# Optimization experiments

Hardware: AMD Instinct MI355X
Metric: run time of the kernel (lower is better)

Reference implementation:

```python
import jax, jax.numpy as jnp
import numpy as np

C = 1.0                 # ball curvature magnitude (k = -c)
SQRT_C = float(np.sqrt(C))
MIN_NORM = 1e-15
BALL_EPS = 4e-3         # geoopt float32 projection eps


def _artanh(x):
    return jnp.arctanh(jnp.clip(x, -1.0 + 1e-7, 1.0 - 1e-7))


def _norm(x):
    return jnp.clip(jnp.linalg.norm(x, axis=-1, keepdims=True), MIN_NORM)


def expmap0(u):
    n = _norm(u)
    return jnp.tanh(SQRT_C * n) * u / (SQRT_C * n)


def logmap0(y):
    n = _norm(y)
    return _artanh(SQRT_C * n) * y / (SQRT_C * n)


def mobius_add(x, y):
    x2 = jnp.sum(x * x, axis=-1, keepdims=True)
    y2 = jnp.sum(y * y, axis=-1, keepdims=True)
    xy = jnp.sum(x * y, axis=-1, keepdims=True)
    num = (1.0 + 2.0 * C * xy + C * y2) * x + (1.0 - C * x2) * y
    den = 1.0 + 2.0 * C * xy + C * C * x2 * y2
    return num / jnp.clip(den, MIN_NORM)


def mobius_matvec(W, x):
    # x: [N, in], W: [out, in]
    mx = x @ W.T                                   # [N, out]
    xn = _norm(x)
    mxn = _norm(mx)
    res = jnp.tanh(mxn / xn * _artanh(SQRT_C * xn)) * mx / (mxn * SQRT_C)
    zero = jnp.linalg.norm(mx, axis=-1, keepdims=True) <= 1e-10
    return jnp.where(zero, jnp.zeros_like(res), res)


def project(x):
    n = _norm(x)
    maxnorm = (1.0 - BALL_EPS) / SQRT_C
    return jnp.where(n > maxnorm, x * (maxnorm / n), x)


def setup_inputs() -> dict:
    key = jax.random.key(0)
    k1, k2, k3, k4, k5 = jax.random.split(key, 5)
    N, E, D_IN, D_OUT = 100000, 600000, 128, 128
    x_h = jax.random.normal(k1, (N, D_IN), dtype=jnp.float32) * 0.05  # inside ball
    edge_index = jax.random.randint(k2, (2, E), 0, N, dtype=jnp.int64)
    edge_weight = jax.random.uniform(k3, (E,), dtype=jnp.float32)
    xav = float(np.sqrt(2.0 / (D_IN + D_OUT)))
    W = jax.random.normal(k4, (D_OUT, D_IN), dtype=jnp.float32) * xav
    b = jax.random.normal(k5, (D_OUT,), dtype=jnp.float32) * 0.01
    a = jnp.asarray(0.25, dtype=jnp.float32)  # PReLU slope
    return {"x_h": x_h, "edge_index": edge_index, "edge_weight": edge_weight,
            "W": W, "b": b, "a": a}


def reference(x_h, edge_index, edge_weight, W, b, a):
    N = x_h.shape[0]
    # HyperbolicLinear: mobius matvec + mobius bias add
    h = mobius_matvec(W, x_h)
    h = mobius_add(h, expmap0(b))
    # tangent-space aggregation
    h_t = logmap0(h)                                  # [N, D]
    src, dst = edge_index[0], edge_index[1]
    msg = h_t[src] * edge_weight[:, None]             # [E, D]
    agg = jax.ops.segment_sum(msg, dst, num_segments=N) + h_t
    # mobius PReLU activation
    h2_t = logmap0(expmap0(agg))
    h2_t = jnp.where(h2_t >= 0, h2_t, a * h2_t)
    return project(expmap0(h2_t))
```

## Files before the change

### kernel.cpp

```cpp
#include <hip/hip_runtime.h>
#include <hip/hip_fp16.h>
#include <cstdint>

#define D 128
#define BLK 256

constexpr float MINN    = 1e-15f;
constexpr float ATCLIP  = 1.0f - 1e-7f;
constexpr float BALLEPS = 4e-3f;

typedef _Float16 f16x8 __attribute__((ext_vector_type(8)));
typedef float    f32x4 __attribute__((ext_vector_type(4)));

union H4 { _Float16 h[4]; uint2 u2; };
union H8 { _Float16 h[8]; uint4 u4; };

__device__ __forceinline__ float red32(float v) {
    v += __shfl_xor(v, 1);
    v += __shfl_xor(v, 2);
    v += __shfl_xor(v, 4);
    v += __shfl_xor(v, 8);
    v += __shfl_xor(v, 16);
    return v;
}

__device__ __forceinline__ float red64(float v) {
    v += __shfl_xor(v, 1, 64);
    v += __shfl_xor(v, 2, 64);
    v += __shfl_xor(v, 4, 64);
    v += __shfl_xor(v, 8, 64);
    v += __shfl_xor(v, 16, 64);
    v += __shfl_xor(v, 32, 64);
    return v;
}

__device__ __forceinline__ float red16(float v) {
    v += __shfl_xor(v, 1, 64);
    v += __shfl_xor(v, 2, 64);
    v += __shfl_xor(v, 4, 64);
    v += __shfl_xor(v, 8, 64);
    return v;
}

__device__ __forceinline__ float tanh_fast(float x) {
    float e = __expf(2.f * fminf(x, 15.f));
    return __fdividef(e - 1.f, e + 1.f);
}
__device__ __forceinline__ float artanh_fast(float x) {
    x = fminf(x, ATCLIP);
    return 0.5f * __logf(__fdividef(1.f + x, 1.f - x));
}

__global__ __launch_bounds__(BLK) void k_node_mfma(
    const float* __restrict__ x, const float* __restrict__ W,
    const float* __restrict__ b, uint2* __restrict__ ht, int N,
    const int* __restrict__ ei, int* __restrict__ cnt, int E, int eslice)
{
    __shared__ _Float16 Ws[D * 136];
    __shared__ _Float16 xs[64 * 136];
    __shared__ float    ps[D];
    __shared__ float    xn2s[64];

    const int t     = threadIdx.x;
    const int node0 = blockIdx.x * 64;

    {
        int e0 = blockIdx.x * eslice;
        for (int i = t; i < eslice; i += BLK) {
            int e = e0 + i;
            if (e < E) atomicAdd(&cnt[ei[E + e]], 1);
        }
    }

    for (int it = 0; it < 16; ++it) {
        int lin = it * BLK + t;
        int row = lin >> 5;
        int c4  = (lin & 31) * 4;
        float4 v = ((const float4*)W)[lin];
        H4 u;
        u.h[0] = (_Float16)v.x; u.h[1] = (_Float16)v.y;
        u.h[2] = (_Float16)v.z; u.h[3] = (_Float16)v.w;
        *(uint2*)&Ws[row * 136 + c4] = u.u2;
    }

    for (int it = 0; it < 8; ++it) {
        int lin  = it * BLK + t;
        int node = lin >> 5;
        int c4   = (lin & 31) * 4;
        int gn   = node0 + node;
        float4 v = make_float4(0.f, 0.f, 0.f, 0.f);
        if (gn < N) v = ((const float4*)x)[(size_t)gn * 32 + (lin & 31)];
        H4 u;
        u.h[0] = (_Float16)v.x; u.h[1] = (_Float16)v.y;
        u.h[2] = (_Float16)v.z; u.h[3] = (_Float16)v.w;
        *(uint2*)&xs[node * 136 + c4] = u.u2;
        float s = fmaf(v.x, v.x, fmaf(v.y, v.y, fmaf(v.z, v.z, v.w * v.w)));
        s = red32(s);
        if ((t & 31) == 0) xn2s[node] = s;
    }

    {
        float2 b2 = ((const float2*)b)[t & 63];
        float pb  = fmaf(b2.x, b2.x, b2.y * b2.y);
        float bn2 = red64(pb);
        float bnc    = fmaxf(sqrtf(bn2), MINN);
        float bscale = __fdividef(tanh_fast(bnc), bnc);
        if (t < D) ps[t] = b[t] * bscale;
        xn2s[0] = xn2s[0];
        __syncthreads();
        const int lane = t & 63;
        const int w    = t >> 6;
        const int c    = lane & 15;
        const int g    = lane >> 4;
        const float y2 = bscale * bscale * bn2;

        f32x4 Cf[8];
#pragma unroll
        for (int mt = 0; mt < 8; ++mt) Cf[mt] = (f32x4){0.f, 0.f, 0.f, 0.f};

        const _Float16* xbase = &xs[(w * 16 + c) * 136];
#pragma unroll
        for (int s = 0; s < 4; ++s) {
            f16x8 Bf = *(const f16x8*)&xbase[s * 32 + g * 8];
#pragma unroll
            for (int mt = 0; mt < 8; ++mt) {
                f16x8 Af = *(const f16x8*)&Ws[(mt * 16 + c) * 136 + s * 32 + g * 8];
                Cf[mt] = __builtin_amdgcn_mfma_f32_16x16x32_f16(Af, Bf, Cf[mt], 0, 0, 0);
            }
        }

        float pm = 0.f, pd = 0.f;
        const float4* ps4 = (const float4*)ps;
#pragma unroll
        for (int mt = 0; mt < 8; ++mt) {
            float4 pv = ps4[mt * 4 + g];
            pm = fmaf(Cf[mt][0], Cf[mt][0], pm);
            pm = fmaf(Cf[mt][1], Cf[mt][1], pm);
            pm = fmaf(Cf[mt][2], Cf[mt][2], pm);
            pm = fmaf(Cf[mt][3], Cf[mt][3], pm);
            pd = fmaf(Cf[mt][0], pv.x, pd);
            pd = fmaf(Cf[mt][1], pv.y, pd);
            pd = fmaf(Cf[mt][2], pv.z, pd);
            pd = fmaf(Cf[mt][3], pv.w, pd);
        }
        pm += __shfl_xor(pm, 16); pm += __shfl_xor(pm, 32);
        pd += __shfl_xor(pd, 16); pd += __shfl_xor(pd, 32);
        float xn2 = xn2s[w * 16 + c];

        float xn      = fmaxf(sqrtf(xn2), MINN);
        float mxn_raw = sqrtf(pm);
        float mxn     = fmaxf(mxn_raw, MINN);
        float alpha   = __fdividef(tanh_fast(__fdividef(mxn, xn) * artanh_fast(xn)), mxn);
        if (mxn_raw <= 1e-10f) alpha = 0.f;

        float x2  = alpha * alpha * pm;
        float xy  = alpha * pd;
        float den = fmaxf(fmaf(x2, y2, 1.f + 2.f * xy), MINN);
        float ca  = __fdividef((1.f + 2.f * xy + y2) * alpha, den);
        float cb  = __fdividef(1.f - x2, den);

        float hn2 = ca * ca * pm + 2.f * ca * cb * pd + cb * cb * y2;
        float hn  = fmaxf(sqrtf(hn2), MINN);
        float lsc = __fdividef(artanh_fast(hn), hn);
        float s1  = lsc * ca, s2 = lsc * cb;

        uint2* lout = (uint2*)((char*)xs + (size_t)w * 16 * 136 * 2);
#pragma unroll
        for (int mt = 0; mt < 8; ++mt) {
            float4 pv = ps4[mt * 4 + g];
            H4 u;
            u.h[0] = (_Float16)fmaf(s1, Cf[mt][0], s2 * pv.x);
            u.h[1] = (_Float16)fmaf(s1, Cf[mt][1], s2 * pv.y);
            u.h[2] = (_Float16)fmaf(s1, Cf[mt][2], s2 * pv.z);
            u.h[3] = (_Float16)fmaf(s1, Cf[mt][3], s2 * pv.w);
            lout[c * 33 + mt * 4 + g] = u.u2;
        }
    }
    __syncthreads();

    for (int it = 0; it < 8; ++it) {
        int lin  = it * BLK + t;
        int node = lin >> 5;
        int col  = lin & 31;
        int gn   = node0 + node;
        if (gn < N) {
            const uint2* lsrc = (const uint2*)((const char*)xs + (size_t)(node >> 4) * 4352);
            ht[(size_t)gn * 32 + col] = lsrc[(node & 15) * 33 + col];
        }
    }
}

__global__ __launch_bounds__(256) void k_scan1(
    const int* __restrict__ cnt, int* __restrict__ ptr,
    int* __restrict__ part, int N)
{
    __shared__ int s[256];
    int t = threadIdx.x;
    int base = blockIdx.x * 1024 + t * 4;
    int v0 = 0, v1 = 0, v2 = 0, v3 = 0;
    if (base + 3 < N) {
        int4 q = *(const int4*)&cnt[base];
        v0 = q.x; v1 = q.y; v2 = q.z; v3 = q.w;
    } else {
        if (base + 0 < N) v0 = cnt[base + 0];
        if (base + 1 < N) v1 = cnt[base + 1];
        if (base + 2 < N) v2 = cnt[base + 2];
        if (base + 3 < N) v3 = cnt[base + 3];
    }
    int sum = v0 + v1 + v2 + v3;
    s[t] = sum;
    __syncthreads();
    for (int off = 1; off < 256; off <<= 1) {
        int xv = (t >= off) ? s[t - off] : 0;
        __syncthreads();
        s[t] += xv;
        __syncthreads();
    }
    int excl = s[t] - sum;
    if (t == 255) part[blockIdx.x] = s[255];
    int r = excl;
    if (base + 0 < N) ptr[base + 0] = r; r += v0;
    if (base + 1 < N) ptr[base + 1] = r; r += v1;
    if (base + 2 < N) ptr[base + 2] = r; r += v2;
    if (base + 3 < N) ptr[base + 3] = r;
}

__global__ __launch_bounds__(256) void k_scan2(int* __restrict__ part, int nc) {
    __shared__ int s[256];
    int t = threadIdx.x;
    int v = (t < nc) ? part[t] : 0;
    s[t] = v;
    __syncthreads();
    for (int off = 1; off < 256; off <<= 1) {
        int xv = (t >= off) ? s[t - off] : 0;
        __syncthreads();
        s[t] += xv;
        __syncthreads();
    }
    if (t < nc) part[t] = s[t] - v;
}

__global__ void k_scatter(const int* __restrict__ ei, const float* __restrict__ ew,
                          int* __restrict__ ptr, const int* __restrict__ part,
                          int2* __restrict__ sorted, int E)
{
    int e = blockIdx.x * 256 + threadIdx.x;
    if (e >= E) return;
    int src = ei[e];
    int dst = ei[E + e];
    float w = ew[e];
    int pos = atomicAdd(&ptr[dst], 1) + part[dst >> 10];
    sorted[pos] = make_int2(src << 8, __float_as_int(w));
}

__global__ __launch_bounds__(256) void k_agg_final(
    const char* __restrict__ htb, const int* __restrict__ ptr,
    const int* __restrict__ part, const int2* __restrict__ sorted,
    const float* __restrict__ a_in, float* __restrict__ out, int N)
{
    const int t   = threadIdx.x;
    const int li  = t & 15;
    const int grp = t >> 4;
    const int n   = blockIdx.x * 16 + grp;
    if (n >= N) return;
    const float a = a_in[0];

    H8 own; own.u4 = *(const uint4*)(htb + (size_t)n * 256 + li * 16);
    float acc[8];
#pragma unroll
    for (int k = 0; k < 8; ++k) acc[k] = (float)own.h[k];

    int s0 = (n > 0) ? (ptr[n - 1] + part[(n - 1) >> 10]) : 0;
    int e0 = ptr[n] + part[n >> 10];

    const int lioff = li * 16;
    int j = s0;
    for (; j + 2 <= e0; j += 2) {
        int2 d0 = sorted[j];
        int2 d1 = sorted[j + 1];
        H8 g0, g1;
        g0.u4 = *(const uint4*)(htb + (unsigned)d0.x + lioff);
        g1.u4 = *(const uint4*)(htb + (unsigned)d1.x + lioff);
        float w0 = __int_as_float(d0.y);
        float w1 = __int_as_float(d1.y);
#pragma unroll
        for (int k = 0; k < 8; ++k) acc[k] = fmaf((float)g0.h[k], w0, acc[k]);
#pragma unroll
        for (int k = 0; k < 8; ++k) acc[k] = fmaf((float)g1.h[k], w1, acc[k]);
    }
    if (j < e0) {
        int2 d = sorted[j];
        H8 g; g.u4 = *(const uint4*)(htb + (unsigned)d.x + lioff);
        float w = __int_as_float(d.y);
#pragma unroll
        for (int k = 0; k < 8; ++k) acc[k] = fmaf((float)g.h[k], w, acc[k]);
    }

    float pv = 0.f;
#pragma unroll
    for (int k = 0; k < 8; ++k) {
        float v = acc[k];
        v = (v >= 0.f) ? v : a * v;
        acc[k] = v;
        pv = fmaf(v, v, pv);
    }
    float m2 = red16(pv);
    float rc = fmaxf(sqrtf(m2), MINN);
    float te = tanh_fast(rc);
    const float maxn = 1.0f - BALLEPS;
    float fsc = __fdividef(fminf(fmaxf(te, MINN), maxn), rc);

    float4 o0 = make_float4(fsc * acc[0], fsc * acc[1], fsc * acc[2], fsc * acc[3]);
    float4 o1 = make_float4(fsc * acc[4], fsc * acc[5], fsc * acc[6], fsc * acc[7]);
    float4* orow = (float4*)(out + (size_t)n * D);
    orow[li * 2 + 0] = o0;
    orow[li * 2 + 1] = o1;
}

extern "C" void kernel_launch(void* const* d_in, const int* in_sizes, int n_in,
                              void* d_out, int out_size, void* d_ws, size_t ws_size,
                              hipStream_t stream)
{
    const float* x  = (const float*)d_in[0];
    const int*   ei = (const int*)  d_in[1];
    const float* ew = (const float*)d_in[2];
    const float* W  = (const float*)d_in[3];
    const float* b  = (const float*)d_in[4];
    const float* a  = (const float*)d_in[5];
    float* out = (float*)d_out;

    const int N = in_sizes[0] / D;
    const int E = in_sizes[1] / 2;

    char* ws = (char*)d_ws;
    size_t HT_B   = (size_t)N * D * 2;
    uint2* ht     = (uint2*)ws;
    int*   cnt    = (int*)(ws + HT_B);
    int*   ptr    = (int*)(ws + HT_B + (size_t)N * 4);
    int*   part   = (int*)(ws + HT_B + (size_t)N * 8);
    int2*  sorted = (int2*)(ws + HT_B + (size_t)N * 8 + 1024);

    int nc  = (N + 1023) / 1024;
    int nb1 = (N + 63) / 64;
    int eslice = (E + nb1 - 1) / nb1;

    hipMemsetAsync(cnt, 0, (size_t)N * 4, stream);
    k_node_mfma<<<nb1, BLK, 0, stream>>>(x, W, b, ht, N, ei, cnt, E, eslice);
    k_scan1<<<nc, 256, 0, stream>>>(cnt, ptr, part, N);
    k_scan2<<<1, 256, 0, stream>>>(part, nc);
    k_scatter<<<(E + 255) / 256, 256, 0, stream>>>(ei, ew, ptr, part, sorted, E);
    k_agg_final<<<(N + 15) / 16, 256, 0, stream>>>((const char*)ht, ptr, part, sorted, a, out, N);
}
```

Baseline: 228.6 us.

## Pre-convert W to fp16 in MFMA fragment layout and read it from global

Adds a small kernel that converts W to fp16 once per call, stored in the per-lane MFMA A-fragment order. The node kernel then stops staging W into LDS in every block and loads the A fragments straight from global memory, where they should stay cached in L2. This drops 34 KB of LDS per block, which may raise occupancy, and removes the repeated per-block convert and store. In exchange it adds an extra kernel launch and global loads inside the MFMA loop.

Result: faster. 220.9 us (-3.4%).

```diff
diff --git a/kernel.cpp b/kernel.cpp
--- a/kernel.cpp
+++ b/kernel.cpp
@@ -51,12 +51,26 @@
     return 0.5f * __logf(__fdividef(1.f + x, 1.f - x));
 }
 
+__global__ void k_wcvt(const float* __restrict__ W, _Float16* __restrict__ Wh) {
+    int i = blockIdx.x * 256 + threadIdx.x;
+    if (i >= 2048) return;
+    int f = i >> 7;
+    int r = i & 127;
+    const float4* src = (const float4*)(W + r * 128 + f * 8);
+    float4 v0 = src[0], v1 = src[1];
+    H8 u;
+    u.h[0] = (_Float16)v0.x; u.h[1] = (_Float16)v0.y;
+    u.h[2] = (_Float16)v0.z; u.h[3] = (_Float16)v0.w;
+    u.h[4] = (_Float16)v1.x; u.h[5] = (_Float16)v1.y;
+    u.h[6] = (_Float16)v1.z; u.h[7] = (_Float16)v1.w;
+    *(uint4*)(Wh + i * 8) = u.u4;
+}
+
 __global__ __launch_bounds__(BLK) void k_node_mfma(
-    const float* __restrict__ x, const float* __restrict__ W,
+    const float* __restrict__ x, const _Float16* __restrict__ Wh,
     const float* __restrict__ b, uint2* __restrict__ ht, int N,
     const int* __restrict__ ei, int* __restrict__ cnt, int E, int eslice)
 {
-    __shared__ _Float16 Ws[D * 136];
     __shared__ _Float16 xs[64 * 136];
     __shared__ float    ps[D];
     __shared__ float    xn2s[64];
@@ -70,17 +84,6 @@
             int e = e0 + i;
             if (e < E) atomicAdd(&cnt[ei[E + e]], 1);
         }
-    }
-
-    for (int it = 0; it < 16; ++it) {
-        int lin = it * BLK + t;
-        int row = lin >> 5;
-        int c4  = (lin & 31) * 4;
-        float4 v = ((const float4*)W)[lin];
-        H4 u;
-        u.h[0] = (_Float16)v.x; u.h[1] = (_Float16)v.y;
-        u.h[2] = (_Float16)v.z; u.h[3] = (_Float16)v.w;
-        *(uint2*)&Ws[row * 136 + c4] = u.u2;
     }
 
     for (int it = 0; it < 8; ++it) {
@@ -99,82 +102,81 @@
         if ((t & 31) == 0) xn2s[node] = s;
     }
 
-    {
-        float2 b2 = ((const float2*)b)[t & 63];
-        float pb  = fmaf(b2.x, b2.x, b2.y * b2.y);
-        float bn2 = red64(pb);
-        float bnc    = fmaxf(sqrtf(bn2), MINN);
-        float bscale = __fdividef(tanh_fast(bnc), bnc);
-        if (t < D) ps[t] = b[t] * bscale;
-        xn2s[0] = xn2s[0];
-        __syncthreads();
-        const int lane = t & 63;
-        const int w    = t >> 6;
-        const int c    = lane & 15;
-        const int g    = lane >> 4;
-        const float y2 = bscale * bscale * bn2;
-
-        f32x4 Cf[8];
-#pragma unroll
-        for (int mt = 0; mt < 8; ++mt) Cf[mt] = (f32x4){0.f, 0.f, 0.f, 0.f};
-
-        const _Float16* xbase = &xs[(w * 16 + c) * 136];
-#pragma unroll
-        for (int s = 0; s < 4; ++s) {
-            f16x8 Bf = *(const f16x8*)&xbase[s * 32 + g * 8];
-#pragma unroll
-            for (int mt = 0; mt < 8; ++mt) {
-                f16x8 Af = *(const f16x8*)&Ws[(mt * 16 + c) * 136 + s * 32 + g * 8];
-                Cf[mt] = __builtin_amdgcn_mfma_f32_16x16x32_f16(Af, Bf, Cf[mt], 0, 0, 0);
-            }
+    float2 b2 = ((const float2*)b)[t & 63];
+    float pb  = fmaf(b2.x, b2.x, b2.y * b2.y);
+    float bn2 = red64(pb);
+    float bnc    = fmaxf(sqrtf(bn2), MINN);
+    float bscale = __fdividef(tanh_fast(bnc), bnc);
+    if (t < D) ps[t] = b[t] * bscale;
+    const float y2 = bscale * bscale * bn2;
+    __syncthreads();
+
+    const int lane = t & 63;
+    const int w    = t >> 6;
+    const int c    = lane & 15;
+    const int g    = lane >> 4;
+
+    f32x4 Cf[8];
+#pragma unroll
+    for (int mt = 0; mt < 8; ++mt) Cf[mt] = (f32x4){0.f, 0.f, 0.f, 0.f};
+
+    const _Float16* xbase = &xs[(w * 16 + c) * 136];
+#pragma unroll
+    for (int s = 0; s < 4; ++s) {
+        f16x8 Bf = *(const f16x8*)&xbase[s * 32 + g * 8];
+        const _Float16* wp = Wh + ((s * 4 + g) << 10) + (c << 3);
+#pragma unroll
+        for (int mt = 0; mt < 8; ++mt) {
+            f16x8 Af = *(const f16x8*)&wp[mt << 7];
+            Cf[mt] = __builtin_amdgcn_mfma_f32_16x16x32_f16(Af, Bf, Cf[mt], 0, 0, 0);
         }
-
-        float pm = 0.f, pd = 0.f;
-        const float4* ps4 = (const float4*)ps;
-#pragma unroll
-        for (int mt = 0; mt < 8; ++mt) {
-            float4 pv = ps4[mt * 4 + g];
-            pm = fmaf(Cf[mt][0], Cf[mt][0], pm);
-            pm = fmaf(Cf[mt][1], Cf[mt][1], pm);
-            pm = fmaf(Cf[mt][2], Cf[mt][2], pm);
-            pm = fmaf(Cf[mt][3], Cf[mt][3], pm);
-            pd = fmaf(Cf[mt][0], pv.x, pd);
-            pd = fmaf(Cf[mt][1], pv.y, pd);
-            pd = fmaf(Cf[mt][2], pv.z, pd);
-            pd = fmaf(Cf[mt][3], pv.w, pd);
-        }
-        pm += __shfl_xor(pm, 16); pm += __shfl_xor(pm, 32);
-        pd += __shfl_xor(pd, 16); pd += __shfl_xor(pd, 32);
-        float xn2 = xn2s[w * 16 + c];
-
-        float xn      = fmaxf(sqrtf(xn2), MINN);
-        float mxn_raw = sqrtf(pm);
-        float mxn     = fmaxf(mxn_raw, MINN);
-        float alpha   = __fdividef(tanh_fast(__fdividef(mxn, xn) * artanh_fast(xn)), mxn);
-        if (mxn_raw <= 1e-10f) alpha = 0.f;
-
-        float x2  = alpha * alpha * pm;
-        float xy  = alpha * pd;
-        float den = fmaxf(fmaf(x2, y2, 1.f + 2.f * xy), MINN);
-        float ca  = __fdividef((1.f + 2.f * xy + y2) * alpha, den);
-        float cb  = __fdividef(1.f - x2, den);
-
-        float hn2 = ca * ca * pm + 2.f * ca * cb * pd + cb * cb * y2;
-        float hn  = fmaxf(sqrtf(hn2), MINN);
-        float lsc = __fdividef(artanh_fast(hn), hn);
-        float s1  = lsc * ca, s2 = lsc * cb;
-
-        uint2* lout = (uint2*)((char*)xs + (size_t)w * 16 * 136 * 2);
-#pragma unroll
-        for (int mt = 0; mt < 8; ++mt) {
-            float4 pv = ps4[mt * 4 + g];
-            H4 u;
-            u.h[0] = (_Float16)fmaf(s1, Cf[mt][0], s2 * pv.x);
-            u.h[1] = (_Float16)fmaf(s1, Cf[mt][1], s2 * pv.y);
-            u.h[2] = (_Float16)fmaf(s1, Cf[mt][2], s2 * pv.z);
-            u.h[3] = (_Float16)fmaf(s1, Cf[mt][3], s2 * pv.w);
-            lout[c * 33 + mt * 4 + g] = u.u2;
-        }
+    }
+
+    float pm = 0.f, pd = 0.f;
+    const float4* ps4 = (const float4*)ps;
+#pragma unroll
+    for (int mt = 0; mt < 8; ++mt) {
+        float4 pv = ps4[mt * 4 + g];
+        pm = fmaf(Cf[mt][0], Cf[mt][0], pm);
+        pm = fmaf(Cf[mt][1], Cf[mt][1], pm);
+        pm = fmaf(Cf[mt][2], Cf[mt][2], pm);
+        pm = fmaf(Cf[mt][3], Cf[mt][3], pm);
+        pd = fmaf(Cf[mt][0], pv.x, pd);
+        pd = fmaf(Cf[mt][1], pv.y, pd);
+        pd = fmaf(Cf[mt][2], pv.z, pd);
+        pd = fmaf(Cf[mt][3], pv.w, pd);
+    }
+    pm += __shfl_xor(pm, 16); pm += __shfl_xor(pm, 32);
+    pd += __shfl_xor(pd, 16); pd += __shfl_xor(pd, 32);
+    float xn2 = xn2s[w * 16 + c];
+
+    float xn      = fmaxf(sqrtf(xn2), MINN);
+    float mxn_raw = sqrtf(pm);
+    float mxn     = fmaxf(mxn_raw, MINN);
+    float alpha   = __fdividef(tanh_fast(__fdividef(mxn, xn) * artanh_fast(xn)), mxn);
+    if (mxn_raw <= 1e-10f) alpha = 0.f;
+
+    float x2  = alpha * alpha * pm;
+    float xy  = alpha * pd;
+    float den = fmaxf(fmaf(x2, y2, 1.f + 2.f * xy), MINN);
+    float ca  = __fdividef((1.f + 2.f * xy + y2) * alpha, den);
+    float cb  = __fdividef(1.f - x2, den);
+
+    float hn2 = ca * ca * pm + 2.f * ca * cb * pd + cb * cb * y2;
+    float hn  = fmaxf(sqrtf(hn2), MINN);
+    float lsc = __fdividef(artanh_fast(hn), hn);
+    float s1  = lsc * ca, s2 = lsc * cb;
+
+    uint2* lout = (uint2*)((char*)xs + (size_t)w * 16 * 136 * 2);
+#pragma unroll
+    for (int mt = 0; mt < 8; ++mt) {
+        float4 pv = ps4[mt * 4 + g];
+        H4 u;
+        u.h[0] = (_Float16)fmaf(s1, Cf[mt][0], s2 * pv.x);
+        u.h[1] = (_Float16)fmaf(s1, Cf[mt][1], s2 * pv.y);
+        u.h[2] = (_Float16)fmaf(s1, Cf[mt][2], s2 * pv.z);
+        u.h[3] = (_Float16)fmaf(s1, Cf[mt][3], s2 * pv.w);
+        lout[c * 33 + mt * 4 + g] = u.u2;
     }
     __syncthreads();
 
@@ -333,19 +335,21 @@
     const int E = in_sizes[1] / 2;
 
     char* ws = (char*)d_ws;
-    size_t HT_B   = (size_t)N * D * 2;
-    uint2* ht     = (uint2*)ws;
-    int*   cnt    = (int*)(ws + HT_B);
-    int*   ptr    = (int*)(ws + HT_B + (size_t)N * 4);
-    int*   part   = (int*)(ws + HT_B + (size_t)N * 8);
-    int2*  sorted = (int2*)(ws + HT_B + (size_t)N * 8 + 1024);
+    size_t HT_B    = (size_t)N * D * 2;
+    uint2*     ht     = (uint2*)ws;
+    int*       cnt    = (int*)(ws + HT_B);
+    int*       ptr    = (int*)(ws + HT_B + (size_t)N * 4);
+    int*       part   = (int*)(ws + HT_B + (size_t)N * 8);
+    int2*      sorted = (int2*)(ws + HT_B + (size_t)N * 8 + 1024);
+    _Float16*  Wh     = (_Float16*)(ws + HT_B + (size_t)N * 8 + 1024 + (size_t)E * 8);
 
     int nc  = (N + 1023) / 1024;
     int nb1 = (N + 63) / 64;
     int eslice = (E + nb1 - 1) / nb1;
 
     hipMemsetAsync(cnt, 0, (size_t)N * 4, stream);
-    k_node_mfma<<<nb1, BLK, 0, stream>>>(x, W, b, ht, N, ei, cnt, E, eslice);
+    k_wcvt<<<8, 256, 0, stream>>>(W, Wh);
+    k_node_mfma<<<nb1, BLK, 0, stream>>>(x, Wh, b, ht, N, ei, cnt, E, eslice);
     k_scan1<<<nc, 256, 0, stream>>>(cnt, ptr, part, N);
     k_scan2<<<1, 256, 0, stream>>>(part, nc);
     k_scatter<<<(E + 255) / 256, 256, 0, stream>>>(ei, ew, ptr, part, sorted, E);
```
